# Kernel tuning notes

Hardware: AMD Instinct MI355X
Metric: run time of the kernel (lower is better)

## Reference

```python
import jax, jax.numpy as jnp
import numpy as np
import math

D_MODEL = 256
SIGMA = 1.0


def _sinusoidal_pe(L, d_model, dtype=jnp.float32):
    # pe[l, 2i] = sin(l * w_i), pe[l, 2i+1] = cos(l * w_i)
    position = jnp.arange(L, dtype=dtype)[:, None]                       # [L,1]
    div_term = jnp.exp(jnp.arange(0, d_model, 2, dtype=dtype) * (-math.log(10000.0) / d_model))
    pe = jnp.zeros((L, d_model), dtype=dtype)
    pe = pe.at[:, 0::2].set(jnp.sin(position * div_term))
    pe = pe.at[:, 1::2].set(jnp.cos(position * div_term))
    return pe  # [L, d_model]


def setup_inputs() -> dict:
    key = jax.random.key(0)
    # scale 0.05 keeps pairwise sq-distances O(1) so S = exp(-d/2) is non-degenerate
    x = jax.random.normal(key, (4, 4096, 256), dtype=jnp.float32) * 0.05
    return {"x": x}


def reference(x):
    B, L, D = x.shape
    pe = _sinusoidal_pe(L, D_MODEL, dtype=x.dtype)[None]                 # [1,L,D]
    # pairwise squared distances via the expansion ||a||^2+||b||^2-2ab (avoids [B,L,L,D])
    sq = jnp.sum(x * x, axis=-1)                                         # [B,L]
    gram = jnp.einsum('bld,bmd->blm', x, x)                              # [B,L,L]
    dist_sq = jnp.maximum(sq[:, :, None] + sq[:, None, :] - 2.0 * gram, 0.0)
    S = jnp.exp(-dist_sq / (2.0 * SIGMA ** 2))                           # [B,L,L]
    sem = jnp.einsum('blm,bmd->bld', S, x) / jnp.sum(S, axis=-1, keepdims=True)
    return x + pe + sem
```

## Files before the change

### kernel.cpp

```cpp
#include <hip/hip_runtime.h>

typedef unsigned char u8;
typedef float f32x4 __attribute__((ext_vector_type(4)));
typedef float f32x16 __attribute__((ext_vector_type(16)));

#define LL 4096
#define PSTR 136
#define SCALE 16.0f
#define GSCALE (1.0f/256.0f)
#define FREQC (-0.03597789207803197f)

__device__ __forceinline__ long LCAST(uint2 v) { return __builtin_bit_cast(long, v); }

typedef __attribute__((address_space(3))) u8 lds_u8;
typedef __attribute__((address_space(1))) u8 glb_u8;
__device__ __forceinline__ void dma16(const u8* g, u8* l) {
  __builtin_amdgcn_global_load_lds((const glb_u8*)g, (lds_u8*)l, 16, 0, 0);
}

__global__ __launch_bounds__(256) void prep1(const float* __restrict__ x, u8* __restrict__ xbf,
                                             u8* __restrict__ xT, float* __restrict__ sq) {
  __shared__ u8 T[16 * 264];
  const int blk = blockIdx.x;
  const int b = blk >> 8, r0 = (blk & 255) << 4;
  const int tid = threadIdx.x;
  const long rowbase = (long)(b << 12) + r0;
  const float4* x4 = (const float4*)x + rowbase * 64;
  unsigned* xb4 = (unsigned*)xbf + rowbase * 64;
  #pragma unroll
  for (int i = 0; i < 4; ++i) {
    int idx = i * 256 + tid;
    float4 v = x4[idx];
    float s = v.x * v.x + v.y * v.y + v.z * v.z + v.w * v.w;
    #pragma unroll
    for (int o = 32; o; o >>= 1) s += __shfl_xor(s, o);
    int row = idx >> 6, dw = idx & 63;
    if ((tid & 63) == 0) sq[rowbase + row] = s;
    int pk = __builtin_amdgcn_cvt_pk_fp8_f32(v.x * SCALE, v.y * SCALE, 0, false);
    pk = __builtin_amdgcn_cvt_pk_fp8_f32(v.z * SCALE, v.w * SCALE, pk, true);
    int sdw = (((dw >> 1) ^ ((r0 + row) & 31)) << 1) | (dw & 1);
    xb4[row * 64 + sdw] = (unsigned)pk;
    *(unsigned*)(T + row * 264 + dw * 4) = (unsigned)pk;
  }
  __syncthreads();
  unsigned ob[4];
  #pragma unroll
  for (int jj = 0; jj < 4; ++jj) {
    unsigned b0 = T[(4 * jj + 0) * 264 + tid];
    unsigned b1 = T[(4 * jj + 1) * 264 + tid];
    unsigned b2 = T[(4 * jj + 2) * 264 + tid];
    unsigned b3 = T[(4 * jj + 3) * 264 + tid];
    ob[jj] = b0 | (b1 << 8) | (b2 << 16) | (b3 << 24);
  }
  u8* drow = xT + ((((long)(b << 8) + tid) << 12)) + ((r0 >> 7) << 7);
  const int cb = (r0 & 127) >> 3, key = tid & 15;
  *(uint2*)(drow + ((cb ^ key) << 3)) = *(uint2*)(ob);
  *(uint2*)(drow + (((cb + 1) ^ key) << 3)) = *(uint2*)(ob + 2);
}

__global__ __launch_bounds__(512, 2) void tpe_main(
    const u8* __restrict__ xbf, const u8* __restrict__ xT,
    const float* __restrict__ sqv,
    const float* __restrict__ x, float* __restrict__ out) {
  __shared__ u8 Kt[2][32768];
  __shared__ u8 Ps[2][64 * PSTR];
  __shared__ float lred[8][64];
  __shared__ float linv[64];

  const int tid = threadIdx.x;
  const int w = tid >> 6;
  const int lane = tid & 63;
  const int l15 = lane & 15, l31 = lane & 31;
  const int q4 = lane >> 4;
  const int q2 = lane >> 5;

  const int blk = blockIdx.x;
  const int b = (blk & 7) >> 1;
  const int qt = ((blk >> 3) << 1) | (blk & 1);
  const int q0 = qt << 6;
  const long bL = (long)b * LL;

  uint2 qf[4][8];
  float qa[4];
  #pragma unroll
  for (int t = 0; t < 4; ++t) {
    const int row = q0 + 16 * t + l15;
    const u8* qrow = xbf + ((bL + row) << 8);
    const int key = row & 31;
    #pragma unroll
    for (int s = 0; s < 8; ++s)
      qf[t][s] = *(const uint2*)(qrow + (((q4 + 4 * s) ^ key) << 3));
    qa[t] = -0.5f * sqv[bL + row];
  }

  f32x16 oacc[2];
  #pragma unroll
  for (int rb = 0; rb < 2; ++rb)
    #pragma unroll
    for (int k = 0; k < 16; ++k) oacc[rb][k] = 0.f;
  float rsacc[4] = {0.f, 0.f, 0.f, 0.f};

  const u8* kbat = xbf + (bL << 8);
  const u8* vseg = xT + (((long)(b << 8) + 32 * w + l31) << 12);
  const int vkey = l31 & 15;

  uint2 vfA[8], vfB[8];

  #pragma unroll
  for (int c = 0; c < 4; ++c) {
    int off = c * 8192 + tid * 16;
    dma16(kbat + off, Kt[0] + off);
  }
  __syncthreads();

#define TPE_ITER(IT, KCUR, KNXT, PPREV, PCUR, VFC, VFN)                                     \
  {                                                                                         \
    const int j0 = (IT) << 7;                                                               \
    if ((IT) < 31) {    \
      const u8* ks = kbat + ((long)((IT) + 1) << 15);                                       \
      _Pragma("unroll")                                                                     \
      for (int c = 0; c < 4; ++c) {                                                         \
        int off = c * 8192 + tid * 16;                                                      \
        dma16(ks + off, (KNXT) + off);                                                      \
      }                                                                                     \
    }                                                                                       \
    float4 skv4 = *(const float4*)(sqv + bL + j0 + 16 * w + 4 * q4);                        \
    if ((IT) != 0) {           \
      _Pragma("unroll")                                                                     \
      for (int s = 0; s < 8; ++s) {                                                         \
        long a0 = *(const long*)((PPREV) + l31 * PSTR + 16 * s + 8 * q2);                   \
        long a1 = *(const long*)((PPREV) + (32 + l31) * PSTR + 16 * s + 8 * q2);            \
        long bv = LCAST(VFC[s]);                                                            \
        oacc[0] = __builtin_amdgcn_mfma_f32_32x32x16_fp8_fp8(a0, bv, oacc[0], 0, 0, 0);     \
        oacc[1] = __builtin_amdgcn_mfma_f32_32x32x16_fp8_fp8(a1, bv, oacc[1], 0, 0, 0);     \
      }                                                                                     \
    }                                                                                       \
    _Pragma("unroll")              \
    for (int s = 0; s < 8; ++s)                                                             \
      VFN[s] = *(const uint2*)(vseg + j0 + (((2 * s + q2) ^ vkey) << 3));                   \
    {                        \
      const int krow = 16 * w + l15;                                                        \
      const int kkey = krow & 31;                                                           \
      const u8* kb2 = (KCUR) + krow * 256;                                                  \
      f32x4 sacc[4];                                                                        \
      _Pragma("unroll")                                                                     \
      for (int t = 0; t < 4; ++t) {                                                         \
        sacc[t][0] = 0.f; sacc[t][1] = 0.f; sacc[t][2] = 0.f; sacc[t][3] = 0.f;             \
      }                                                                                     \
      _Pragma("unroll")                                                                     \
      for (int s = 0; s < 8; ++s) {                                                         \
        uint2 kf = *(const uint2*)(kb2 + (((q4 + 4 * s) ^ kkey) << 3));                     \
        long av = LCAST(kf);                                                                \
        _Pragma("unroll")                                                                   \
        for (int t = 0; t < 4; ++t)                                                         \
          sacc[t] = __builtin_amdgcn_mfma_f32_16x16x32_fp8_fp8(av, LCAST(qf[t][s]), sacc[t], 0, 0, 0); \
      }                                                                                     \
      _Pragma("unroll")        \
      for (int t = 0; t < 4; ++t) {                 \
        float p0 = __expf(fminf(fmaf(sacc[t][0], GSCALE, qa[t] + skv4.x), 0.f));            \
        float p1 = __expf(fminf(fmaf(sacc[t][1], GSCALE, qa[t] + skv4.y), 0.f));            \
        float p2 = __expf(fminf(fmaf(sacc[t][2], GSCALE, qa[t] + skv4.z), 0.f));            \
        float p3 = __expf(fminf(fmaf(sacc[t][3], GSCALE, qa[t] + skv4.w), 0.f));            \
        rsacc[t] += (p0 + p1) + (p2 + p3);                                                  \
        int pk = __builtin_amdgcn_cvt_pk_fp8_f32(p0, p1, 0, false);                         \
        pk = __builtin_amdgcn_cvt_pk_fp8_f32(p2, p3, pk, true);                             \
        *(int*)((PCUR) + (16 * t + l15) * PSTR + 16 * w + 4 * q4) = pk;                     \
      }                                                                                     \
    }                                                                                       \
    __syncthreads();         \
  }

  for (int it2 = 0; it2 < 16; ++it2) {
    TPE_ITER(2 * it2,     Kt[0], Kt[1], Ps[1], Ps[0], vfA, vfB)
    TPE_ITER(2 * it2 + 1, Kt[1], Kt[0], Ps[0], Ps[1], vfB, vfA)
  }
#undef TPE_ITER

  #pragma unroll
  for (int s = 0; s < 8; ++s) {
    long a0 = *(const long*)(Ps[1] + l31 * PSTR + 16 * s + 8 * q2);
    long a1 = *(const long*)(Ps[1] + (32 + l31) * PSTR + 16 * s + 8 * q2);
    long bv = LCAST(vfA[s]);
    oacc[0] = __builtin_amdgcn_mfma_f32_32x32x16_fp8_fp8(a0, bv, oacc[0], 0, 0, 0);
    oacc[1] = __builtin_amdgcn_mfma_f32_32x32x16_fp8_fp8(a1, bv, oacc[1], 0, 0, 0);
  }

  #pragma unroll
  for (int t = 0; t < 4; ++t) {
    float r = rsacc[t];
    r += __shfl_xor(r, 16);
    r += __shfl_xor(r, 32);
    if (lane < 16) lred[w][16 * t + l15] = r;
  }
  __syncthreads();
  if (tid < 64) {
    float s = 0.f;
    #pragma unroll
    for (int ww = 0; ww < 8; ++ww) s += lred[ww][tid];
    linv[tid] = 0.0625f / s;
  }
  __syncthreads();
  const int col = 32 * w + l31;
  const float freq = __expf((float)(col & ~1) * FREQC);
  #pragma unroll
  for (int rb = 0; rb < 2; ++rb) {
    #pragma unroll
    for (int reg = 0; reg < 16; ++reg) {
      int row = 32 * rb + 4 * q2 + (reg & 3) + 8 * (reg >> 2);
      int l = q0 + row;
      float ang = (float)l * freq;
      float pv = (col & 1) ? __cosf(ang) : __sinf(ang);
      long off = ((bL + l) << 8) + col;
      out[off] = oacc[rb][reg] * linv[row] + x[off] + pv;
    }
  }
}

extern "C" void kernel_launch(void* const* d_in, const int* in_sizes, int n_in,
                              void* d_out, int out_size, void* d_ws, size_t ws_size,
                              hipStream_t stream) {
  const float* x = (const float*)d_in[0];
  float* out = (float*)d_out;
  char* ws = (char*)d_ws;
  u8* xbf = (u8*)ws;
  u8* xT = (u8*)(ws + 4194304);
  float* sq = (float*)(ws + 8388608);
  prep1<<<1024, 256, 0, stream>>>(x, xbf, xT, sq);
  tpe_main<<<256, 512, 0, stream>>>(xbf, xT, sq, x, out);
}
```

Measured before the change: 139.7 us.

## Specialize warps into QK/softmax and PV groups with 1024-thread blocks

```diff
diff --git a/kernel.cpp b/kernel.cpp
--- a/kernel.cpp
+++ b/kernel.cpp
@@ -7,7 +7,8 @@
 #define LL 4096
 #define PSTR 136
 #define SCALE 16.0f
-#define GSCALE (1.0f/256.0f)
+#define GSCALE2 (1.44269504f/256.0f)
+#define NHL2E (-0.721347520444482f)
 #define FREQC (-0.03597789207803197f)
 
 __device__ __forceinline__ long LCAST(uint2 v) { return __builtin_bit_cast(long, v); }
@@ -35,7 +36,7 @@
     #pragma unroll
     for (int o = 32; o; o >>= 1) s += __shfl_xor(s, o);
     int row = idx >> 6, dw = idx & 63;
-    if ((tid & 63) == 0) sq[rowbase + row] = s;
+    if ((tid & 63) == 0) sq[rowbase + row] = s * NHL2E;
     int pk = __builtin_amdgcn_cvt_pk_fp8_f32(v.x * SCALE, v.y * SCALE, 0, false);
     pk = __builtin_amdgcn_cvt_pk_fp8_f32(v.z * SCALE, v.w * SCALE, pk, true);
     int sdw = (((dw >> 1) ^ ((r0 + row) & 31)) << 1) | (dw & 1);
@@ -58,10 +59,11 @@
   *(uint2*)(drow + (((cb + 1) ^ key) << 3)) = *(uint2*)(ob + 2);
 }
 
-__global__ __launch_bounds__(512, 2) void tpe_main(
+__global__ __launch_bounds__(1024, 4) void tpe_main(
     const u8* __restrict__ xbf, const u8* __restrict__ xT,
-    const float* __restrict__ sqv,
+    const float* __restrict__ sqh,
     const float* __restrict__ x, float* __restrict__ out) {
+  __shared__ u8 Qs[16384];
   __shared__ u8 Kt[2][32768];
   __shared__ u8 Ps[2][64 * PSTR];
   __shared__ float lred[8][64];
@@ -80,117 +82,119 @@
   const int q0 = qt << 6;
   const long bL = (long)b * LL;
 
-  uint2 qf[4][8];
+  const u8* kbat = xbf + (bL << 8);
+  const u8* vseg = xT + (((long)(b << 8) + 32 * (w & 7) + l31) << 12);
+  const int vkey = l31 & 15;
+
+  dma16(kbat + (q0 << 8) + tid * 16, Qs + tid * 16);
+  if (w < 8) {
+    #pragma unroll
+    for (int c = 0; c < 4; ++c) {
+      int off = c * 8192 + tid * 16;
+      dma16(kbat + off, Kt[0] + off);
+    }
+  }
+
   float qa[4];
-  #pragma unroll
-  for (int t = 0; t < 4; ++t) {
-    const int row = q0 + 16 * t + l15;
-    const u8* qrow = xbf + ((bL + row) << 8);
-    const int key = row & 31;
-    #pragma unroll
-    for (int s = 0; s < 8; ++s)
-      qf[t][s] = *(const uint2*)(qrow + (((q4 + 4 * s) ^ key) << 3));
-    qa[t] = -0.5f * sqv[bL + row];
-  }
-
+  if (w < 8) {
+    #pragma unroll
+    for (int t = 0; t < 4; ++t) qa[t] = sqh[bL + q0 + 16 * t + l15];
+  }
   f32x16 oacc[2];
   #pragma unroll
   for (int rb = 0; rb < 2; ++rb)
     #pragma unroll
     for (int k = 0; k < 16; ++k) oacc[rb][k] = 0.f;
   float rsacc[4] = {0.f, 0.f, 0.f, 0.f};
-
-  const u8* kbat = xbf + (bL << 8);
-  const u8* vseg = xT + (((long)(b << 8) + 32 * w + l31) << 12);
-  const int vkey = l31 & 15;
-
   uint2 vfA[8], vfB[8];
 
-  #pragma unroll
-  for (int c = 0; c < 4; ++c) {
-    int off = c * 8192 + tid * 16;
-    dma16(kbat + off, Kt[0] + off);
-  }
-  __syncthreads();
-
-#define TPE_ITER(IT, KCUR, KNXT, PPREV, PCUR, VFC, VFN)                                     \
+  __syncthreads();
+
+#define TPE_ITER(IT, KCUR, KNXT, PCUR, PPREV, VFN, VFC)                                     \
   {                                                                                         \
-    const int j0 = (IT) << 7;                                                               \
-    if ((IT) < 31) {    \
-      const u8* ks = kbat + ((long)((IT) + 1) << 15);                                       \
-      _Pragma("unroll")                                                                     \
-      for (int c = 0; c < 4; ++c) {                                                         \
-        int off = c * 8192 + tid * 16;                                                      \
-        dma16(ks + off, (KNXT) + off);                                                      \
-      }                                                                                     \
-    }                                                                                       \
-    float4 skv4 = *(const float4*)(sqv + bL + j0 + 16 * w + 4 * q4);                        \
-    if ((IT) != 0) {           \
-      _Pragma("unroll")                                                                     \
-      for (int s = 0; s < 8; ++s) {                                                         \
-        long a0 = *(const long*)((PPREV) + l31 * PSTR + 16 * s + 8 * q2);                   \
-        long a1 = *(const long*)((PPREV) + (32 + l31) * PSTR + 16 * s + 8 * q2);            \
-        long bv = LCAST(VFC[s]);                                                            \
-        oacc[0] = __builtin_amdgcn_mfma_f32_32x32x16_fp8_fp8(a0, bv, oacc[0], 0, 0, 0);     \
-        oacc[1] = __builtin_amdgcn_mfma_f32_32x32x16_fp8_fp8(a1, bv, oacc[1], 0, 0, 0);     \
-      }                                                                                     \
-    }                                                                                       \
-    _Pragma("unroll")              \
-    for (int s = 0; s < 8; ++s)                                                             \
-      VFN[s] = *(const uint2*)(vseg + j0 + (((2 * s + q2) ^ vkey) << 3));                   \
-    {                        \
-      const int krow = 16 * w + l15;                                                        \
-      const int kkey = krow & 31;                                                           \
-      const u8* kb2 = (KCUR) + krow * 256;                                                  \
+    if (w < 8) {                                                                            \
+      if ((IT) < 31) {        \
+        const u8* ks = kbat + ((long)((IT) + 1) << 15);                                     \
+        _Pragma("unroll")                                                                   \
+        for (int c = 0; c < 4; ++c) {                                                       \
+          int off = c * 8192 + tid * 16;                                                    \
+          dma16(ks + off, (KNXT) + off);                                                    \
+        }                                                                                   \
+      }                                                                                     \
+      float4 skv4 = *(const float4*)(sqh + bL + ((IT) << 7) + 16 * w + 4 * q4);             \
       f32x4 sacc[4];                                                                        \
       _Pragma("unroll")                                                                     \
       for (int t = 0; t < 4; ++t) {                                                         \
         sacc[t][0] = 0.f; sacc[t][1] = 0.f; sacc[t][2] = 0.f; sacc[t][3] = 0.f;             \
       }                                                                                     \
+      const int krow = 16 * w + l15;                                                        \
+      const int kkey = krow & 31;                                                           \
+      const u8* kb2 = (KCUR) + krow * 256;                                                  \
       _Pragma("unroll")                                                                     \
-      for (int s = 0; s < 8; ++s) {                                                         \
-        uint2 kf = *(const uint2*)(kb2 + (((q4 + 4 * s) ^ kkey) << 3));                     \
-        long av = LCAST(kf);                                                                \
+      for (int s = 0; s < 8; ++s) {             \
+        long av = *(const long*)(kb2 + (((q4 + 4 * s) ^ kkey) << 3));                       \
         _Pragma("unroll")                                                                   \
-        for (int t = 0; t < 4; ++t)                                                         \
-          sacc[t] = __builtin_amdgcn_mfma_f32_16x16x32_fp8_fp8(av, LCAST(qf[t][s]), sacc[t], 0, 0, 0); \
-      }                                                                                     \
-      _Pragma("unroll")        \
+        for (int t = 0; t < 4; ++t) {                                                       \
+          const int qrow = 16 * t + l15;                                                    \
+          long qv = *(const long*)(Qs + qrow * 256 + (((q4 + 4 * s) ^ (qrow & 31)) << 3));  \
+          sacc[t] = __builtin_amdgcn_mfma_f32_16x16x32_fp8_fp8(av, qv, sacc[t], 0, 0, 0);   \
+        }                                                                                   \
+      }                                                                                     \
+      _Pragma("unroll")                  \
       for (int t = 0; t < 4; ++t) {                 \
-        float p0 = __expf(fminf(fmaf(sacc[t][0], GSCALE, qa[t] + skv4.x), 0.f));            \
-        float p1 = __expf(fminf(fmaf(sacc[t][1], GSCALE, qa[t] + skv4.y), 0.f));            \
-        float p2 = __expf(fminf(fmaf(sacc[t][2], GSCALE, qa[t] + skv4.z), 0.f));            \
-        float p3 = __expf(fminf(fmaf(sacc[t][3], GSCALE, qa[t] + skv4.w), 0.f));            \
+        float p0 = __builtin_amdgcn_exp2f(fminf(fmaf(sacc[t][0], GSCALE2, qa[t] + skv4.x), 0.f)); \
+        float p1 = __builtin_amdgcn_exp2f(fminf(fmaf(sacc[t][1], GSCALE2, qa[t] + skv4.y), 0.f)); \
+        float p2 = __builtin_amdgcn_exp2f(fminf(fmaf(sacc[t][2], GSCALE2, qa[t] + skv4.z), 0.f)); \
+        float p3 = __builtin_amdgcn_exp2f(fminf(fmaf(sacc[t][3], GSCALE2, qa[t] + skv4.w), 0.f)); \
         rsacc[t] += (p0 + p1) + (p2 + p3);                                                  \
         int pk = __builtin_amdgcn_cvt_pk_fp8_f32(p0, p1, 0, false);                         \
         pk = __builtin_amdgcn_cvt_pk_fp8_f32(p2, p3, pk, true);                             \
         *(int*)((PCUR) + (16 * t + l15) * PSTR + 16 * w + 4 * q4) = pk;                     \
       }                                                                                     \
+    } else {                                                                                \
+      const int j0 = (IT) << 7;                                                             \
+      _Pragma("unroll")                                  \
+      for (int s = 0; s < 8; ++s)                                                           \
+        VFN[s] = *(const uint2*)(vseg + j0 + (((2 * s + q2) ^ vkey) << 3));                 \
+      if ((IT) != 0) {            \
+        _Pragma("unroll")                                                                   \
+        for (int s = 0; s < 8; ++s) {                                                       \
+          long a0 = *(const long*)((PPREV) + l31 * PSTR + 16 * s + 8 * q2);                 \
+          long a1 = *(const long*)((PPREV) + (32 + l31) * PSTR + 16 * s + 8 * q2);          \
+          long bv = LCAST(VFC[s]);                                                          \
+          oacc[0] = __builtin_amdgcn_mfma_f32_32x32x16_fp8_fp8(a0, bv, oacc[0], 0, 0, 0);   \
+          oacc[1] = __builtin_amdgcn_mfma_f32_32x32x16_fp8_fp8(a1, bv, oacc[1], 0, 0, 0);   \
+        }                                                                                   \
+      }                                                                                     \
     }                                                                                       \
-    __syncthreads();         \
+    __syncthreads();                \
   }
 
   for (int it2 = 0; it2 < 16; ++it2) {
-    TPE_ITER(2 * it2,     Kt[0], Kt[1], Ps[1], Ps[0], vfA, vfB)
-    TPE_ITER(2 * it2 + 1, Kt[1], Kt[0], Ps[0], Ps[1], vfB, vfA)
+    TPE_ITER(2 * it2,     Kt[0], Kt[1], Ps[0], Ps[1], vfA, vfB)
+    TPE_ITER(2 * it2 + 1, Kt[1], Kt[0], Ps[1], Ps[0], vfB, vfA)
   }
 #undef TPE_ITER
 
-  #pragma unroll
-  for (int s = 0; s < 8; ++s) {
-    long a0 = *(const long*)(Ps[1] + l31 * PSTR + 16 * s + 8 * q2);
-    long a1 = *(const long*)(Ps[1] + (32 + l31) * PSTR + 16 * s + 8 * q2);
-    long bv = LCAST(vfA[s]);
-    oacc[0] = __builtin_amdgcn_mfma_f32_32x32x16_fp8_fp8(a0, bv, oacc[0], 0, 0, 0);
-    oacc[1] = __builtin_amdgcn_mfma_f32_32x32x16_fp8_fp8(a1, bv, oacc[1], 0, 0, 0);
-  }
-
-  #pragma unroll
-  for (int t = 0; t < 4; ++t) {
-    float r = rsacc[t];
-    r += __shfl_xor(r, 16);
-    r += __shfl_xor(r, 32);
-    if (lane < 16) lred[w][16 * t + l15] = r;
+  if (w >= 8) {
+    #pragma unroll
+    for (int s = 0; s < 8; ++s) {
+      long a0 = *(const long*)(Ps[1] + l31 * PSTR + 16 * s + 8 * q2);
+      long a1 = *(const long*)(Ps[1] + (32 + l31) * PSTR + 16 * s + 8 * q2);
+      long bv = LCAST(vfB[s]);
+      oacc[0] = __builtin_amdgcn_mfma_f32_32x32x16_fp8_fp8(a0, bv, oacc[0], 0, 0, 0);
+      oacc[1] = __builtin_amdgcn_mfma_f32_32x32x16_fp8_fp8(a1, bv, oacc[1], 0, 0, 0);
+    }
+  }
+
+  if (w < 8) {
+    #pragma unroll
+    for (int t = 0; t < 4; ++t) {
+      float r = rsacc[t];
+      r += __shfl_xor(r, 16);
+      r += __shfl_xor(r, 32);
+      if (lane < 16) lred[w][16 * t + l15] = r;
+    }
   }
   __syncthreads();
   if (tid < 64) {
@@ -200,18 +204,20 @@
     linv[tid] = 0.0625f / s;
   }
   __syncthreads();
-  const int col = 32 * w + l31;
-  const float freq = __expf((float)(col & ~1) * FREQC);
-  #pragma unroll
-  for (int rb = 0; rb < 2; ++rb) {
-    #pragma unroll
-    for (int reg = 0; reg < 16; ++reg) {
-      int row = 32 * rb + 4 * q2 + (reg & 3) + 8 * (reg >> 2);
-      int l = q0 + row;
-      float ang = (float)l * freq;
-      float pv = (col & 1) ? __cosf(ang) : __sinf(ang);
-      long off = ((bL + l) << 8) + col;
-      out[off] = oacc[rb][reg] * linv[row] + x[off] + pv;
+  if (w >= 8) {
+    const int col = 32 * (w & 7) + l31;
+    const float freq = __expf((float)(col & ~1) * FREQC);
+    #pragma unroll
+    for (int rb = 0; rb < 2; ++rb) {
+      #pragma unroll
+      for (int reg = 0; reg < 16; ++reg) {
+        int row = 32 * rb + 4 * q2 + (reg & 3) + 8 * (reg >> 2);
+        int l = q0 + row;
+        float ang = (float)l * freq;
+        float pv = (col & 1) ? __cosf(ang) : __sinf(ang);
+        long off = ((bL + l) << 8) + col;
+        out[off] = oacc[rb][reg] * linv[row] + x[off] + pv;
+      }
     }
   }
 }
@@ -226,5 +232,5 @@
   u8* xT = (u8*)(ws + 4194304);
   float* sq = (float*)(ws + 8388608);
   prep1<<<1024, 256, 0, stream>>>(x, xbf, xT, sq);
-  tpe_main<<<256, 512, 0, stream>>>(xbf, xT, sq, x, out);
-}
+  tpe_main<<<256, 1024, 0, stream>>>(xbf, xT, sq, x, out);
+}
```

After: 417.4 us. 2.99x slower.
